# Kernel tuning notes

Hardware: AMD Instinct MI355X
Metric: run time of the kernel (lower is better)

The kernel has to match this reference:

```python
import jax, jax.numpy as jnp
import numpy as np

DECAY = 0.99
EPS_VQ = 1e-5
EPS_LN = 1e-5


def setup_inputs() -> dict:
    key = jax.random.key(0)
    ks = jax.random.split(key, 6)
    N, DIN, D, K = 32768, 1024, 512, 1024
    return {
        "x": jax.random.normal(ks[0], (N, DIN), dtype=jnp.float32),
        "enc_w": jax.random.normal(ks[1], (DIN, D), dtype=jnp.float32) * (1.0 / np.sqrt(DIN)),
        "enc_b": jnp.zeros((D,), jnp.float32),
        "ln_g": jnp.ones((D,), jnp.float32),
        "ln_b": jnp.zeros((D,), jnp.float32),
        "dec_w": jax.random.normal(ks[2], (D, DIN), dtype=jnp.float32) * (1.0 / np.sqrt(D)),
        "dec_b": jnp.zeros((DIN,), jnp.float32),
        "embeddings": jax.random.normal(ks[3], (K, D), dtype=jnp.float32),
        "cluster_size": jnp.ones((K,), jnp.float32),
        "ema_embed_sum": jax.random.normal(ks[4], (K, D), dtype=jnp.float32),
    }


def _layernorm(h, g, b):
    mu = jnp.mean(h, axis=-1, keepdims=True)
    var = jnp.var(h, axis=-1, keepdims=True)
    return (h - mu) * jax.lax.rsqrt(var + EPS_LN) * g + b


def reference(x, enc_w, enc_b, ln_g, ln_b, dec_w, dec_b, embeddings, cluster_size, ema_embed_sum):
    K = embeddings.shape[0]
    # encoder: Linear + LayerNorm
    z_e = _layernorm(x @ enc_w + enc_b, ln_g, ln_b)  # [N, D]
    # pairwise squared L2 distances, expanded GEMM form (same argmin as (z-e)^2.sum)
    d = (jnp.sum(z_e * z_e, axis=1, keepdims=True)
         - 2.0 * (z_e @ embeddings.T)
         + jnp.sum(embeddings * embeddings, axis=1)[None, :])  # [N, K]
    indices = jnp.argmin(d, axis=1)  # [N]
    z_q = embeddings[indices]  # gather [N, D]
    # EMA codebook update (training path; buffers, no grad)
    zd = jax.lax.stop_gradient(z_e)
    counts = jax.ops.segment_sum(jnp.ones_like(indices, jnp.float32), indices, num_segments=K)
    embed_sum = jax.ops.segment_sum(zd, indices, num_segments=K)  # one_hot.T @ z
    new_cluster_size = DECAY * cluster_size + (1.0 - DECAY) * counts
    new_ema_embed_sum = DECAY * ema_embed_sum + (1.0 - DECAY) * embed_sum
    n = jnp.sum(new_cluster_size)
    cs = (new_cluster_size + EPS_VQ) / (n + K * EPS_VQ) * n
    new_embeddings = new_ema_embed_sum / cs[:, None]
    # commitment loss + straight-through estimator
    commit_loss = jnp.mean((z_e - jax.lax.stop_gradient(z_q)) ** 2)
    z_q_st = z_e + jax.lax.stop_gradient(z_q - z_e)
    x_recon = z_q_st @ dec_w + dec_b
    return (x_recon, commit_loss, indices, z_e, z_q_st,
            new_embeddings, new_cluster_size, new_ema_embed_sum)
```

## Files before the change

kernel.cpp:

```cpp
#include <hip/hip_runtime.h>

typedef unsigned long long u64;
typedef unsigned int u32;
typedef _Float16 f16;
typedef _Float16 f16x8 __attribute__((ext_vector_type(8)));
typedef float f32x4 __attribute__((ext_vector_type(4)));

#define MFMA16(a, b, c) __builtin_amdgcn_mfma_f32_16x16x32_f16(a, b, c, 0, 0, 0)

#define NROWS 32768
#define DIN   1024
#define DM    512
#define KC    1024
#define SPLIT_SC  1024.0f
#define SPLIT_INV 0.0009765625f
#define CHSZ  32
#define MAXCH 2048
#define MARGIN 0.5f

#define OFF_XR   0ull
#define OFF_CL   33554432ull
#define OFF_IDX  33554433ull
#define OFF_ZE   33587201ull
#define OFF_ZQ   50364417ull
#define OFF_NE   67141633ull
#define OFF_NCS  67665921ull
#define OFF_NEMA 67666945ull

#define WS_ZNORM   2359296ull
#define WS_IDX     2490368ull
#define WS_COUNTS  2621440ull
#define WS_STARTS  2625536ull
#define WS_OFFW    2629632ull
#define WS_ROWLIST 2633728ull
#define WS_CSD     2764800ull
#define WS_ENORM   2769920ull
#define WS2_CAND   (4ull<<20)
#define WS2_WT1    (36ull<<20)
#define WS2_WT2    (37ull<<20)
#define WS2_DT     (38ull<<20)
#define WS2_E1     (39ull<<20)
#define WS3_CHPFX  (41ull<<20)
#define WS3_CHCODE ((41ull<<20) + 8192)
#define WS3_CPART  ((41ull<<20) + 16384)
#define WS3_PART   ((41ull<<20) + 65536)

__device__ inline void gload16(const f16* g, f16* l) {
  __builtin_amdgcn_global_load_lds((const __attribute__((address_space(1))) void*)g,
                                   (__attribute__((address_space(3))) void*)l, 16, 0, 0);
}

__device__ inline f16x8 ldfrag32(const f16* p, int row, int kc) {
  return *(const f16x8*)(p + row * 32 + ((kc ^ ((row >> 1) & 3)) << 3));
}

__device__ inline void stage32(const f16* gbase, int ld, int row0, int k0,
                               f16* lds, int t) {
  int r = t >> 2, c = t & 3;
  int cs = c ^ ((r >> 1) & 3);
  gload16(gbase + (size_t)(row0 + r) * ld + k0 + cs * 8, lds + t * 8);
}

__device__ inline void stageA256(const f16* gbase, int ld, int row0, int k0,
                                 f16* lds, int t) {
#pragma unroll
  for (int h = 0; h < 2; h++) {
    int e = t + h * 512;
    int r = e >> 2, c = e & 3;
    int cs = c ^ ((r >> 1) & 3);
    gload16(gbase + (size_t)(row0 + r) * ld + k0 + cs * 8, lds + e * 8);
  }
}

__device__ inline u32 enc_score(float s) {
  u32 kb = __float_as_uint(s);
  return (kb & 0x80000000u) ? ~kb : (kb | 0x80000000u);
}
__device__ inline float dec_score(u32 u) {
  u32 b = (u & 0x80000000u) ? (u & 0x7fffffffu) : ~u;
  return __uint_as_float(b);
}

__global__ __launch_bounds__(256) void k_prep(const float* __restrict__ enc_w,
                                              const float* __restrict__ dec_w,
                                              const float* __restrict__ emb,
                                              f16* __restrict__ wt1,
                                              f16* __restrict__ wt2,
                                              f16* __restrict__ dT,
                                              f16* __restrict__ e1,
                                              float* __restrict__ enorm,
                                              int* __restrict__ counts) {
  __shared__ float tile[32][33];
  int bid = blockIdx.x, t = threadIdx.x;
  if (bid < 1024) {
    const float* W;
    f16 *o1, *o2;
    int K, N, bx, by;
    if (bid < 512) {
      W = enc_w; o1 = wt1; o2 = wt2; K = DIN; N = DM;
      bx = bid & 15; by = bid >> 4;
    } else {
      int b2 = bid - 512;
      W = dec_w; o1 = dT; o2 = nullptr; K = DM; N = DIN;
      bx = b2 & 31; by = b2 >> 5;
    }
    int tx = t & 31, ty = t >> 5;
    int nb = bx * 32, kb = by * 32;
#pragma unroll
    for (int i = 0; i < 32; i += 8)
      tile[ty + i][tx] = W[(size_t)(kb + ty + i) * N + nb + tx];
    __syncthreads();
#pragma unroll
    for (int i = 0; i < 32; i += 8) {
      float v = tile[tx][ty + i];
      f16 h = (f16)v;
      size_t o = (size_t)(nb + ty + i) * K + kb + tx;
      o1[o] = h;
      if (o2) o2[o] = (f16)((v - (float)h) * SPLIT_SC);
    }
  } else if (bid < 1536) {
    int tid = (bid - 1024) * 256 + t;
    for (int i = tid; i < KC * DM; i += 131072) e1[i] = (f16)emb[i];
  } else if (bid < 1792) {
    int k = (bid - 1536) * 4 + (t >> 6), lane = t & 63;
    float s = 0.f;
#pragma unroll
    for (int j = 0; j < 8; j++) {
      float v = emb[(size_t)k * DM + lane + j * 64];
      s = fmaf(v, v, s);
    }
#pragma unroll
    for (int m = 1; m < 64; m <<= 1) s += __shfl_xor(s, m, 64);
    if (lane == 0) enorm[k] = s;
  } else {
    int i = (bid - 1792) * 256 + t;
    if (i < KC) counts[i] = 0;
  }
}

__global__ __launch_bounds__(512, 4) void k_genc6(const float* __restrict__ x,
                                                  const f16* __restrict__ wt1,
                                                  const f16* __restrict__ wt2,
                                                  const float* __restrict__ bias,
                                                  float* __restrict__ dst) {
  __shared__ __align__(16) f16 A1[2][128 * 32], A2[2][128 * 32];
  __shared__ __align__(16) f16 B1[2][128 * 32], B2[2][128 * 32];
  int t = threadIdx.x, lane = t & 63, wid = t >> 6;
  int wm = wid >> 2, wn = wid & 3;
  int l = blockIdx.x;
  int xcd = l & 7, s = l >> 3, ct = s & 3;
  int p = ((s >> 2) << 3) | xcd;
  int m0 = p * 128, n0 = ct * 128;
  int r = t >> 2, cg = t & 3;
  int cslot = cg ^ ((r >> 1) & 3);
  const float* ax = x + (size_t)(m0 + r) * DIN + cg * 8;
  f32x4 accA[4][2] = {}, accB[4][2] = {};

#define GCONV(v0, v1, buf)                                                  \
  {                                                                         \
    float a_[8] = {v0.x, v0.y, v0.z, v0.w, v1.x, v1.y, v1.z, v1.w};         \
    f16 h1_[8], h2_[8];                                                     \
    _Pragma("unroll") for (int j_ = 0; j_ < 8; j_++) {                      \
      f16 h_ = (f16)a_[j_];                                                 \
      h1_[j_] = h_;                                                         \
      h2_[j_] = (f16)((a_[j_] - (float)h_) * SPLIT_SC);                     \
    }                                                                       \
    *(f16x8*)(A1[buf] + r * 32 + cslot * 8) = *(f16x8*)h1_;                 \
    *(f16x8*)(A2[buf] + r * 32 + cslot * 8) = *(f16x8*)h2_;                 \
  }

#define GCOMP(buf)                                                          \
  {                                                                         \
    int kc_ = lane >> 4;                                                    \
    f16x8 a1f[4], a2f[4], b1f[2], b2f[2];                                   \
    _Pragma("unroll") for (int m_ = 0; m_ < 4; m_++) {                      \
      int row_ = wm * 64 + m_ * 16 + (lane & 15);                           \
      a1f[m_] = ldfrag32(A1[buf], row_, kc_);                               \
      a2f[m_] = ldfrag32(A2[buf], row_, kc_);                               \
    }                                                                       \
    _Pragma("unroll") for (int n_ = 0; n_ < 2; n_++) {                      \
      int row_ = wn * 32 + n_ * 16 + (lane & 15);                           \
      b1f[n_] = ldfrag32(B1[buf], row_, kc_);                               \
      b2f[n_] = ldfrag32(B2[buf], row_, kc_);                               \
    }                                                                       \
    _Pragma("unroll") for (int m_ = 0; m_ < 4; m_++)                        \
      _Pragma("unroll") for (int n_ = 0; n_ < 2; n_++) {                    \
        accA[m_][n_] = MFMA16(a1f[m_], b1f[n_], accA[m_][n_]);              \
        accB[m_][n_] = MFMA16(a1f[m_], b2f[n_], accB[m_][n_]);              \
        accB[m_][n_] = MFMA16(a2f[m_], b1f[n_], accB[m_][n_]);              \
      }                                                                     \
  }

  float4 c0 = *(const float4*)(ax);
  float4 c1 = *(const float4*)(ax + 4);
  stage32(wt1, DIN, n0, 0, B1[0], t);
  stage32(wt2, DIN, n0, 0, B2[0], t);
  float4 n0v = *(const float4*)(ax + 32);
  float4 n1v = *(const float4*)(ax + 36);
  asm volatile("s_waitcnt vmcnt(4)" ::: "memory");
  GCONV(c0, c1, 0);
  asm volatile("s_waitcnt vmcnt(2) lgkmcnt(0)" ::: "memory");
  __builtin_amdgcn_sched_barrier(0);
  __builtin_amdgcn_s_barrier();
  asm volatile("" ::: "memory");

  for (int it = 0; it < 32; ++it) {
    if (it + 1 < 32) {
      stage32(wt1, DIN, n0, (it + 1) * 32, B1[(it + 1) & 1], t);
      stage32(wt2, DIN, n0, (it + 1) * 32, B2[(it + 1) & 1], t);
    }
    float4 f0, f1;
    if (it + 2 < 32) {
      f0 = *(const float4*)(ax + (it + 2) * 32);
      f1 = *(const float4*)(ax + (it + 2) * 32 + 4);
    }
    GCOMP(it & 1);
    if (it + 1 < 32) {
      if (it <= 29) {
        asm volatile("s_waitcnt vmcnt(4)" ::: "memory");
      } else {
        asm volatile("s_waitcnt vmcnt(2)" ::: "memory");
      }
      GCONV(n0v, n1v, (it + 1) & 1);
      if (it <= 29) {
        asm volatile("s_waitcnt vmcnt(2) lgkmcnt(0)" ::: "memory");
      } else {
        asm volatile("s_waitcnt vmcnt(0) lgkmcnt(0)" ::: "memory");
      }
      __builtin_amdgcn_sched_barrier(0);
      __builtin_amdgcn_s_barrier();
      asm volatile("" ::: "memory");
    }
    n0v = f0; n1v = f1;
  }
#undef GCONV
#undef GCOMP

#pragma unroll
  for (int m = 0; m < 4; m++)
#pragma unroll
    for (int n = 0; n < 2; n++)
#pragma unroll
      for (int j = 0; j < 4; j++) {
        int row = m0 + wm * 64 + m * 16 + (lane >> 4) * 4 + j;
        int col = n0 + wn * 32 + n * 16 + (lane & 15);
        dst[(size_t)row * DM + col] = accA[m][n][j] + SPLIT_INV * accB[m][n][j] + bias[col];
      }
}

__global__ __launch_bounds__(512, 4) void k_dist4(const f16* __restrict__ z1,
                                                  const f16* __restrict__ e1,
                                                  const float* __restrict__ enorm,
                                                  u64* __restrict__ cand) {
  __shared__ __align__(16) f16 A[3][256 * 32];
  __shared__ __align__(16) f16 B[3][128 * 32];
  int t = threadIdx.x, lane = t & 63, wid = t >> 6;
  int wr = wid >> 1, wc = wid & 1;
  int l = blockIdx.x;
  int xcd = l & 7, s = l >> 3, ct = s & 7;
  int p = ((s >> 3) << 3) | xcd;
  int r0 = p * 256, c0 = ct * 128;
  f32x4 acc[4][4] = {};
  int kc = lane >> 4;

  stageA256(z1, DM, r0, 0, A[0], t);
  stage32(e1, DM, c0, 0, B[0], t);

  for (int it = 0; it < 16; ++it) {
    int buf = it % 3;
    if (it < 15) {
      int nb = (it + 1) % 3;
      int k0n = (it + 1) * 32;
      stageA256(z1, DM, r0, k0n, A[nb], t);
      stage32(e1, DM, c0, k0n, B[nb], t);
      asm volatile("s_waitcnt vmcnt(3)" ::: "memory");
    } else {
      asm volatile("s_waitcnt vmcnt(0)" ::: "memory");
    }
    __builtin_amdgcn_sched_barrier(0);
    __builtin_amdgcn_s_barrier();
    asm volatile("" ::: "memory");
    f16x8 af[4], bf[4];
#pragma unroll
    for (int m = 0; m < 4; m++)
      af[m] = ldfrag32(A[buf], wr * 64 + m * 16 + (lane & 15), kc);
#pragma unroll
    for (int n = 0; n < 4; n++)
      bf[n] = ldfrag32(B[buf], wc * 64 + n * 16 + (lane & 15), kc);
#pragma unroll
    for (int m = 0; m < 4; m++)
#pragma unroll
      for (int n = 0; n < 4; n++) acc[m][n] = MFMA16(af[m], bf[n], acc[m][n]);
  }

  __syncthreads();
  u64 (*cand_s)[4] = (u64 (*)[4])(&A[0][0]);
  float en[4];
#pragma unroll
  for (int n = 0; n < 4; n++)
    en[n] = enorm[c0 + wc * 64 + n * 16 + (lane & 15)];
#pragma unroll
  for (int m = 0; m < 4; m++)
#pragma unroll
    for (int j = 0; j < 4; j++) {
      int r_l = wr * 64 + m * 16 + (lane >> 4) * 4 + j;
      u64 lo = ~0ull, hi = ~0ull;
#pragma unroll
      for (int n = 0; n < 4; n++) {
        int col = c0 + wc * 64 + n * 16 + (lane & 15);
        float sc = fmaf(-2.0f, acc[m][n][j], en[n]);
        u64 k = ((u64)enc_score(sc) << 32) | (u32)col;
        if (k < lo) { hi = lo; lo = k; }
        else if (k < hi) { hi = k; }
      }
#pragma unroll
      for (int msk = 1; msk < 16; msk <<= 1) {
        u64 lo2 = __shfl_xor(lo, msk, 64);
        u64 hi2 = __shfl_xor(hi, msk, 64);
        u64 nlo = lo < lo2 ? lo : lo2;
        u64 losr = lo < lo2 ? lo2 : lo;
        u64 nh = hi < hi2 ? hi : hi2;
        hi = losr < nh ? losr : nh;
        lo = nlo;
      }
      if ((lane & 15) == 0) {
        cand_s[r_l][wc * 2] = lo;
        cand_s[r_l][wc * 2 + 1] = hi;
      }
    }
  __syncthreads();
  if (t < 256) {
    u64 b0 = ~0ull, b1 = ~0ull;
#pragma unroll
    for (int i = 0; i < 4; i++) {
      u64 k = cand_s[t][i];
      if (k < b0) { b1 = b0; b0 = k; }
      else if (k < b1) { b1 = k; }
    }
    u64* dst = cand + ((size_t)(r0 + t) * 16 + ct * 2);
    dst[0] = b0;
    dst[1] = b1;
  }
}

__global__ __launch_bounds__(512) void k_edgemm(const f16* __restrict__ e1,
                                                const f16* __restrict__ dT,
                                                const float* __restrict__ bias,
                                                float* __restrict__ ED) {
  __shared__ __align__(16) f16 A[3][128 * 32], B[3][128 * 32];
  int t = threadIdx.x, lane = t & 63, wid = t >> 6;
  int wm = wid >> 2, wn = wid & 3;
  int r0 = (blockIdx.x >> 3) * 128, c0 = (blockIdx.x & 7) * 128;
  f32x4 acc[4][2] = {};
  int kc = lane >> 4;

  stage32(e1, DM, r0, 0, A[0], t);
  stage32(dT, DM, c0, 0, B[0], t);

  for (int it = 0; it < 16; ++it) {
    int buf = it % 3;
    if (it < 15) {
      int nb = (it + 1) % 3;
      int k0n = (it + 1) * 32;
      stage32(e1, DM, r0, k0n, A[nb], t);
      stage32(dT, DM, c0, k0n, B[nb], t);
      asm volatile("s_waitcnt vmcnt(2)" ::: "memory");
    } else {
      asm volatile("s_waitcnt vmcnt(0)" ::: "memory");
    }
    __builtin_amdgcn_sched_barrier(0);
    __builtin_amdgcn_s_barrier();
    asm volatile("" ::: "memory");
    f16x8 af[4], bf[2];
#pragma unroll
    for (int m = 0; m < 4; m++)
      af[m] = ldfrag32(A[buf], wm * 64 + m * 16 + (lane & 15), kc);
#pragma unroll
    for (int n = 0; n < 2; n++)
      bf[n] = ldfrag32(B[buf], wn * 32 + n * 16 + (lane & 15), kc);
#pragma unroll
    for (int m = 0; m < 4; m++)
#pragma unroll
      for (int n = 0; n < 2; n++) acc[m][n] = MFMA16(af[m], bf[n], acc[m][n]);
  }

#pragma unroll
  for (int m = 0; m < 4; m++)
#pragma unroll
    for (int n = 0; n < 2; n++)
#pragma unroll
      for (int j = 0; j < 4; j++) {
        int row = r0 + wm * 64 + m * 16 + (lane >> 4) * 4 + j;
        int col = c0 + wn * 32 + n * 16 + (lane & 15);
        ED[(size_t)row * DIN + col] = acc[m][n][j] + bias[col];
      }
}

__global__ __launch_bounds__(256) void k_gatherx(const int* __restrict__ idxws,
                                                 const float* __restrict__ ED,
                                                 float* __restrict__ xr) {
  int t = threadIdx.x, r0 = blockIdx.x * 16;
  __shared__ int idx_s[16];
  if (t < 16) idx_s[t] = idxws[r0 + t];
  __syncthreads();
  for (int rr = 0; rr < 16; rr++) {
    int R = r0 + rr;
    const float4* src = (const float4*)(ED + (size_t)idx_s[rr] * DIN);
    float4* dst = (float4*)(xr + (size_t)R * DIN);
    dst[t] = src[t];
  }
}

__global__ __launch_bounds__(256) void k_resolve(const u64* __restrict__ cand,
                                                 const float* __restrict__ znorm,
                                                 const float* __restrict__ enorm,
                                                 const float* __restrict__ emb,
                                                 float* __restrict__ out,
                                                 int* __restrict__ idxws,
                                                 int* __restrict__ counts,
                                                 float* __restrict__ cpart) {
  int t = threadIdx.x, bid = blockIdx.x;
  int r0 = bid * 16;
  __shared__ u64 key_s[256];
  __shared__ int idx_s[16];
  __shared__ float commit_s[16];
  __shared__ int flagcnt_s;
  __shared__ int flagrow_s[16];
  key_s[t] = cand[(size_t)r0 * 16 + t];
  if (t == 0) flagcnt_s = 0;
  __syncthreads();

  if (t < 16) {
    u64 best = ~0ull;
#pragma unroll
    for (int i = 0; i < 16; i++) {
      u64 k = key_s[t * 16 + i];
      best = k < best ? k : best;
    }
    float smin = dec_score((u32)(best >> 32));
    float thr = smin + MARGIN;
    int nc = 0;
#pragma unroll
    for (int i = 0; i < 16; i++)
      if (dec_score((u32)(key_s[t * 16 + i] >> 32)) <= thr) nc++;
    idx_s[t] = (int)(u32)(best & 0xffffffffull);
    commit_s[t] = znorm[r0 + t] + smin;
    if (nc > 1) {
      int pz = atomicAdd(&flagcnt_s, 1);
      flagrow_s[pz] = t;
    }
  }
  __syncthreads();

  if (t < 64) {
    int nf = flagcnt_s;
    for (int fi = 0; fi < nf; fi++) {
      int lr = flagrow_s[fi];
      int R = r0 + lr;
      u64 amin = ~0ull;
      for (int i = 0; i < 16; i++) {
        u64 k = key_s[lr * 16 + i];
        amin = k < amin ? k : amin;
      }
      float thr = dec_score((u32)(amin >> 32)) + MARGIN;
      float zn = znorm[R];
      const float* z = out + OFF_ZE + (size_t)R * DM;
      u64 bestk = ~0ull;
      for (int i = 0; i < 16; i++) {
        u64 k = key_s[lr * 16 + i];
        if (dec_score((u32)(k >> 32)) > thr) continue;
        int c = (int)(u32)(k & 0xffffffffull);
        const float* e = emb + (size_t)c * DM;
        float pdot = 0.f;
#pragma unroll
        for (int j = 0; j < 8; j++) pdot = fmaf(z[t + j * 64], e[t + j * 64], pdot);
#pragma unroll
        for (int m = 1; m < 64; m <<= 1) pdot += __shfl_xor(pdot, m, 64);
        float d = fmaf(-2.0f, pdot, zn) + enorm[c];
        u64 pk = ((u64)enc_score(d) << 32) | (u32)c;
        bestk = pk < bestk ? pk : bestk;
      }
      if (t == 0) {
        idx_s[lr] = (int)(u32)(bestk & 0xffffffffull);
        commit_s[lr] = dec_score((u32)(bestk >> 32));
      }
    }
  }
  __syncthreads();

  if (t < 16) {
    int R = r0 + t;
    int idx = idx_s[t];
    out[OFF_IDX + R] = (float)idx;
    idxws[R] = idx;
    atomicAdd(counts + idx, 1);
  }
  __syncthreads();
  for (int rr = 0; rr < 16; rr++) {
    int R = r0 + rr;
    const float* e = emb + (size_t)idx_s[rr] * DM;
    float* zq = out + OFF_ZQ + (size_t)R * DM;
#pragma unroll
    for (int j = 0; j < 2; j++) {
      int c = t + j * 256;
      zq[c] = e[c];
    }
  }
  if (t == 0) {
    float s = 0.f;
#pragma unroll
    for (int i = 0; i < 16; i++) s += commit_s[i];
    cpart[bid] = s;
  }
}

__global__ __launch_bounds__(256) void k_ln3(float* __restrict__ ze,
                                             const float* __restrict__ g,
                                             const float* __restrict__ b,
                                             f16* __restrict__ z1,
                                             float* __restrict__ znorm) {
  int t = threadIdx.x, lane = t & 63, wid = t >> 6;
  int R = blockIdx.x * 4 + wid;
  float* row = ze + (size_t)R * DM;
  float v[8];
  float s = 0.f, sq = 0.f;
#pragma unroll
  for (int j = 0; j < 8; j++) {
    v[j] = row[lane + j * 64];
    s += v[j];
    sq = fmaf(v[j], v[j], sq);
  }
#pragma unroll
  for (int m = 1; m < 64; m <<= 1) {
    s += __shfl_xor(s, m, 64);
    sq += __shfl_xor(sq, m, 64);
  }
  float mu = s * (1.f / DM);
  float var = sq * (1.f / DM) - mu * mu;
  float rs = rsqrtf(var + 1e-5f);
  float zn = 0.f;
#pragma unroll
  for (int j = 0; j < 8; j++) {
    int c = lane + j * 64;
    float o = (v[j] - mu) * rs * g[c] + b[c];
    row[c] = o;
    z1[(size_t)R * DM + c] = (f16)o;
    zn = fmaf(o, o, zn);
  }
#pragma unroll
  for (int m = 1; m < 64; m <<= 1) zn += __shfl_xor(zn, m, 64);
  if (lane == 0) znorm[R] = zn;
}

__global__ __launch_bounds__(1024) void k_scan(const int* __restrict__ counts,
                                               const float* __restrict__ cs_in,
                                               float* __restrict__ out,
                                               int* __restrict__ starts,
                                               int* __restrict__ offw,
                                               float* __restrict__ csd,
                                               const float* __restrict__ cpart,
                                               int* __restrict__ chpfx,
                                               int* __restrict__ chcode) {
  __shared__ float f[1024];
  __shared__ int ib[1024];
  int t = threadIdx.x;
  f[t] = cpart[t] + cpart[t + 1024];
  __syncthreads();
  for (int s = 512; s > 0; s >>= 1) {
    if (t < s) f[t] += f[t + s];
    __syncthreads();
  }
  if (t == 0) out[OFF_CL] = f[0] * (1.f / ((float)NROWS * (float)DM));
  __syncthreads();

  int cnt = counts[t];
  float ncs = 0.99f * cs_in[t] + 0.01f * (float)cnt;
  out[OFF_NCS + t] = ncs;
  f[t] = ncs;
  __syncthreads();
  for (int s = 512; s > 0; s >>= 1) {
    if (t < s) f[t] += f[t + s];
    __syncthreads();
  }
  float n = f[0];
  csd[t] = (ncs + 1e-5f) / (n + (float)KC * 1e-5f) * n;
  ib[t] = cnt;
  __syncthreads();
  for (int s = 1; s < 1024; s <<= 1) {
    int y = (t >= s) ? ib[t - s] : 0;
    __syncthreads();
    ib[t] += y;
    __syncthreads();
  }
  int excl = ib[t] - cnt;
  starts[t] = excl;
  offw[t] = excl;
  int nch = (cnt + CHSZ - 1) / CHSZ;
  __syncthreads();
  ib[t] = nch;
  __syncthreads();
  for (int s = 1; s < 1024; s <<= 1) {
    int y = (t >= s) ? ib[t - s] : 0;
    __syncthreads();
    ib[t] += y;
    __syncthreads();
  }
  int chx = ib[t] - nch;
  chpfx[t] = chx;
  if (t == KC - 1) chpfx[KC] = ib[t];
  for (int j = 0; j < nch; j++) chcode[chx + j] = t;
}

__global__ __launch_bounds__(256) void k_scatter(const int* __restrict__ idxws,
                                                 int* __restrict__ offw,
                                                 int* __restrict__ rowlist) {
  int r = blockIdx.x * 256 + threadIdx.x;
  int idx = idxws[r];
  int pos = atomicAdd(offw + idx, 1);
  rowlist[pos] = r;
}

__global__ __launch_bounds__(128) void k_partsum(const int* __restrict__ chpfx,
                                                 const int* __restrict__ chcode,
                                                 const int* __restrict__ starts,
                                                 const int* __restrict__ counts,
                                                 const int* __restrict__ rowlist,
                                                 const float* __restrict__ out,
                                                 float* __restrict__ part) {
  int c = blockIdx.x, t = threadIdx.x;
  if (c >= chpfx[KC]) return;
  int code = chcode[c];
  int j = c - chpfx[code];
  int ofs = starts[code] + j * CHSZ;
  int len = min(CHSZ, counts[code] - j * CHSZ);
  __shared__ int rl[CHSZ];
  if (t < len) rl[t] = rowlist[ofs + t];
  __syncthreads();
  const float* zeb = out + OFF_ZE;
  float a0 = 0.f, a1 = 0.f, a2 = 0.f, a3 = 0.f;
  for (int i = 0; i < len; i++) {
    const float* z = zeb + (size_t)rl[i] * DM;
    a0 += z[t];
    a1 += z[t + 128];
    a2 += z[t + 256];
    a3 += z[t + 384];
  }
  float* pp = part + (size_t)c * DM;
  pp[t] = a0;
  pp[t + 128] = a1;
  pp[t + 256] = a2;
  pp[t + 384] = a3;
}

__global__ __launch_bounds__(128) void k_codesum2(const int* __restrict__ chpfx,
                                                  const float* __restrict__ part,
                                                  const float* __restrict__ ema_in,
                                                  const float* __restrict__ csd,
                                                  float* __restrict__ out) {
  int k = blockIdx.x, t = threadIdx.x;
  int base = chpfx[k], nch = chpfx[k + 1] - base;
  float a0 = 0.f, a1 = 0.f, a2 = 0.f, a3 = 0.f;
  for (int i = 0; i < nch; i++) {
    const float* pp = part + (size_t)(base + i) * DM;
    a0 += pp[t];
    a1 += pp[t + 128];
    a2 += pp[t + 256];
    a3 += pp[t + 384];
  }
  float cs = csd[k];
  float sum[4] = {a0, a1, a2, a3};
#pragma unroll
  for (int j = 0; j < 4; j++) {
    int c = t + j * 128;
    float e = 0.99f * ema_in[(size_t)k * DM + c] + 0.01f * sum[j];
    out[OFF_NEMA + (size_t)k * DM + c] = e;
    out[OFF_NE + (size_t)k * DM + c] = e / cs;
  }
}

extern "C" void kernel_launch(void* const* d_in, const int* in_sizes, int n_in,
                              void* d_out, int out_size, void* d_ws, size_t ws_size,
                              hipStream_t stream) {
  (void)in_sizes; (void)n_in; (void)out_size; (void)ws_size;
  const float* x = (const float*)d_in[0];
  const float* enc_w = (const float*)d_in[1];
  const float* enc_b = (const float*)d_in[2];
  const float* ln_g = (const float*)d_in[3];
  const float* ln_b = (const float*)d_in[4];
  const float* dec_w = (const float*)d_in[5];
  const float* dec_b = (const float*)d_in[6];
  const float* emb = (const float*)d_in[7];
  const float* cs_in = (const float*)d_in[8];
  const float* ema_in = (const float*)d_in[9];
  float* out = (float*)d_out;
  char* ws = (char*)d_ws;
  float* znorm = (float*)(ws + WS_ZNORM);
  int* idxws = (int*)(ws + WS_IDX);
  int* counts = (int*)(ws + WS_COUNTS);
  int* starts = (int*)(ws + WS_STARTS);
  int* offw = (int*)(ws + WS_OFFW);
  int* rowlist = (int*)(ws + WS_ROWLIST);
  float* csd = (float*)(ws + WS_CSD);
  float* enorm = (float*)(ws + WS_ENORM);
  u64* cand = (u64*)(ws + WS2_CAND);
  float* ED = (float*)(ws + WS2_CAND);
  f16* wt1 = (f16*)(ws + WS2_WT1);
  f16* wt2 = (f16*)(ws + WS2_WT2);
  f16* dT = (f16*)(ws + WS2_DT);
  f16* e1 = (f16*)(ws + WS2_E1);
  int* chpfx = (int*)(ws + WS3_CHPFX);
  int* chcode = (int*)(ws + WS3_CHCODE);
  float* cpart = (float*)(ws + WS3_CPART);
  float* part = (float*)(ws + WS3_PART);
  f16* z1 = (f16*)out;

  k_prep<<<dim3(1796), dim3(256), 0, stream>>>(enc_w, dec_w, emb, wt1, wt2, dT,
                                               e1, enorm, counts);
  k_genc6<<<dim3(1024), dim3(512), 0, stream>>>(x, wt1, wt2, enc_b, out + OFF_ZE);
  k_ln3<<<dim3(8192), dim3(256), 0, stream>>>(out + OFF_ZE, ln_g, ln_b, z1, znorm);
  k_dist4<<<dim3(1024), dim3(512), 0, stream>>>(z1, e1, enorm, cand);
  k_resolve<<<dim3(2048), dim3(256), 0, stream>>>(cand, znorm, enorm, emb, out,
                                                  idxws, counts, cpart);
  k_edgemm<<<dim3(64), dim3(512), 0, stream>>>(e1, dT, dec_b, ED);
  k_scan<<<dim3(1), dim3(1024), 0, stream>>>(counts, cs_in, out, starts, offw, csd,
                                             cpart, chpfx, chcode);
  k_scatter<<<dim3(NROWS / 256), dim3(256), 0, stream>>>(idxws, offw, rowlist);
  k_partsum<<<dim3(MAXCH), dim3(128), 0, stream>>>(chpfx, chcode, starts, counts,
                                                   rowlist, out, part);
  k_codesum2<<<dim3(KC), dim3(128), 0, stream>>>(chpfx, part, ema_in, csd, out);
  k_gatherx<<<dim3(2048), dim3(256), 0, stream>>>(idxws, ED, out + OFF_XR);
}
```

Baseline: 331.7 us.

## Triple-buffer encoder weight tiles and retile distance GEMM to fewer column tiles

The encoder GEMM now triple-buffers the B (weight) tiles, issuing loads two iterations ahead so weight fetches are hidden behind more compute. The distance kernel swaps its tile shape from 256 rows by 128 codes to 128 rows by 256 codes. Each row therefore yields 8 candidate keys instead of 16, and the resolve kernel and scan partial sums are resized to match. This cuts candidate write and read traffic and resolve work. The cost is more LDS per block and a different reuse balance in the distance GEMM.

```diff
diff --git a/kernel.cpp b/kernel.cpp
--- a/kernel.cpp
+++ b/kernel.cpp
@@ -138,13 +138,13 @@
   }
 }
 
-__global__ __launch_bounds__(512, 4) void k_genc6(const float* __restrict__ x,
+__global__ __launch_bounds__(512, 4) void k_genc7(const float* __restrict__ x,
                                                   const f16* __restrict__ wt1,
                                                   const f16* __restrict__ wt2,
                                                   const float* __restrict__ bias,
                                                   float* __restrict__ dst) {
   __shared__ __align__(16) f16 A1[2][128 * 32], A2[2][128 * 32];
-  __shared__ __align__(16) f16 B1[2][128 * 32], B2[2][128 * 32];
+  __shared__ __align__(16) f16 B1[3][128 * 32], B2[3][128 * 32];
   int t = threadIdx.x, lane = t & 63, wid = t >> 6;
   int wm = wid >> 2, wn = wid & 3;
   int l = blockIdx.x;
@@ -169,19 +169,19 @@
     *(f16x8*)(A2[buf] + r * 32 + cslot * 8) = *(f16x8*)h2_;                 \
   }
 
-#define GCOMP(buf)                                                          \
+#define GCOMP(abuf, bbuf)                                                   \
   {                                                                         \
     int kc_ = lane >> 4;                                                    \
     f16x8 a1f[4], a2f[4], b1f[2], b2f[2];                                   \
     _Pragma("unroll") for (int m_ = 0; m_ < 4; m_++) {                      \
       int row_ = wm * 64 + m_ * 16 + (lane & 15);                           \
-      a1f[m_] = ldfrag32(A1[buf], row_, kc_);                               \
-      a2f[m_] = ldfrag32(A2[buf], row_, kc_);                               \
+      a1f[m_] = ldfrag32(A1[abuf], row_, kc_);                              \
+      a2f[m_] = ldfrag32(A2[abuf], row_, kc_);                              \
     }                                                                       \
     _Pragma("unroll") for (int n_ = 0; n_ < 2; n_++) {                      \
       int row_ = wn * 32 + n_ * 16 + (lane & 15);                           \
-      b1f[n_] = ldfrag32(B1[buf], row_, kc_);                               \
-      b2f[n_] = ldfrag32(B2[buf], row_, kc_);                               \
+      b1f[n_] = ldfrag32(B1[bbuf], row_, kc_);                              \
+      b2f[n_] = ldfrag32(B2[bbuf], row_, kc_);                              \
     }                                                                       \
     _Pragma("unroll") for (int m_ = 0; m_ < 4; m_++)                        \
       _Pragma("unroll") for (int n_ = 0; n_ < 2; n_++) {                    \
@@ -191,42 +191,38 @@
       }                                                                     \
   }
 
+  stage32(wt1, DIN, n0, 0, B1[0], t);
+  stage32(wt2, DIN, n0, 0, B2[0], t);
   float4 c0 = *(const float4*)(ax);
   float4 c1 = *(const float4*)(ax + 4);
-  stage32(wt1, DIN, n0, 0, B1[0], t);
-  stage32(wt2, DIN, n0, 0, B2[0], t);
+  stage32(wt1, DIN, n0, 32, B1[1], t);
+  stage32(wt2, DIN, n0, 32, B2[1], t);
   float4 n0v = *(const float4*)(ax + 32);
   float4 n1v = *(const float4*)(ax + 36);
   asm volatile("s_waitcnt vmcnt(4)" ::: "memory");
   GCONV(c0, c1, 0);
-  asm volatile("s_waitcnt vmcnt(2) lgkmcnt(0)" ::: "memory");
+  asm volatile("s_waitcnt lgkmcnt(0)" ::: "memory");
   __builtin_amdgcn_sched_barrier(0);
   __builtin_amdgcn_s_barrier();
   asm volatile("" ::: "memory");
 
   for (int it = 0; it < 32; ++it) {
-    if (it + 1 < 32) {
-      stage32(wt1, DIN, n0, (it + 1) * 32, B1[(it + 1) & 1], t);
-      stage32(wt2, DIN, n0, (it + 1) * 32, B2[(it + 1) & 1], t);
-    }
     float4 f0, f1;
     if (it + 2 < 32) {
+      stage32(wt1, DIN, n0, (it + 2) * 32, B1[(it + 2) % 3], t);
+      stage32(wt2, DIN, n0, (it + 2) * 32, B2[(it + 2) % 3], t);
       f0 = *(const float4*)(ax + (it + 2) * 32);
       f1 = *(const float4*)(ax + (it + 2) * 32 + 4);
     }
-    GCOMP(it & 1);
+    GCOMP(it & 1, it % 3);
     if (it + 1 < 32) {
       if (it <= 29) {
         asm volatile("s_waitcnt vmcnt(4)" ::: "memory");
       } else {
-        asm volatile("s_waitcnt vmcnt(2)" ::: "memory");
+        asm volatile("s_waitcnt vmcnt(0)" ::: "memory");
       }
       GCONV(n0v, n1v, (it + 1) & 1);
-      if (it <= 29) {
-        asm volatile("s_waitcnt vmcnt(2) lgkmcnt(0)" ::: "memory");
-      } else {
-        asm volatile("s_waitcnt vmcnt(0) lgkmcnt(0)" ::: "memory");
-      }
+      asm volatile("s_waitcnt lgkmcnt(0)" ::: "memory");
       __builtin_amdgcn_sched_barrier(0);
       __builtin_amdgcn_s_barrier();
       asm volatile("" ::: "memory");
@@ -248,31 +244,31 @@
       }
 }
 
-__global__ __launch_bounds__(512, 4) void k_dist4(const f16* __restrict__ z1,
+__global__ __launch_bounds__(512, 4) void k_dist5(const f16* __restrict__ z1,
                                                   const f16* __restrict__ e1,
                                                   const float* __restrict__ enorm,
                                                   u64* __restrict__ cand) {
-  __shared__ __align__(16) f16 A[3][256 * 32];
-  __shared__ __align__(16) f16 B[3][128 * 32];
+  __shared__ __align__(16) f16 A[3][128 * 32];
+  __shared__ __align__(16) f16 B[3][256 * 32];
   int t = threadIdx.x, lane = t & 63, wid = t >> 6;
-  int wr = wid >> 1, wc = wid & 1;
+  int wr = wid >> 2, wc = wid & 3;
   int l = blockIdx.x;
-  int xcd = l & 7, s = l >> 3, ct = s & 7;
-  int p = ((s >> 3) << 3) | xcd;
-  int r0 = p * 256, c0 = ct * 128;
+  int xcd = l & 7, s = l >> 3, ct = s & 3;
+  int p = ((s >> 2) << 3) | xcd;
+  int r0 = p * 128, c0 = ct * 256;
   f32x4 acc[4][4] = {};
   int kc = lane >> 4;
 
-  stageA256(z1, DM, r0, 0, A[0], t);
-  stage32(e1, DM, c0, 0, B[0], t);
+  stage32(z1, DM, r0, 0, A[0], t);
+  stageA256(e1, DM, c0, 0, B[0], t);
 
   for (int it = 0; it < 16; ++it) {
     int buf = it % 3;
     if (it < 15) {
       int nb = (it + 1) % 3;
       int k0n = (it + 1) * 32;
-      stageA256(z1, DM, r0, k0n, A[nb], t);
-      stage32(e1, DM, c0, k0n, B[nb], t);
+      stage32(z1, DM, r0, k0n, A[nb], t);
+      stageA256(e1, DM, c0, k0n, B[nb], t);
       asm volatile("s_waitcnt vmcnt(3)" ::: "memory");
     } else {
       asm volatile("s_waitcnt vmcnt(0)" ::: "memory");
@@ -294,7 +290,7 @@
   }
 
   __syncthreads();
-  u64 (*cand_s)[4] = (u64 (*)[4])(&A[0][0]);
+  u64 (*cand_s)[8] = (u64 (*)[8])(&A[0][0]);
   float en[4];
 #pragma unroll
   for (int n = 0; n < 4; n++)
@@ -329,17 +325,120 @@
       }
     }
   __syncthreads();
-  if (t < 256) {
+  if (t < 128) {
     u64 b0 = ~0ull, b1 = ~0ull;
 #pragma unroll
-    for (int i = 0; i < 4; i++) {
+    for (int i = 0; i < 8; i++) {
       u64 k = cand_s[t][i];
       if (k < b0) { b1 = b0; b0 = k; }
       else if (k < b1) { b1 = k; }
     }
-    u64* dst = cand + ((size_t)(r0 + t) * 16 + ct * 2);
+    u64* dst = cand + ((size_t)(r0 + t) * 8 + ct * 2);
     dst[0] = b0;
     dst[1] = b1;
+  }
+}
+
+__global__ __launch_bounds__(256) void k_resolve5(const u64* __restrict__ cand,
+                                                  const float* __restrict__ znorm,
+                                                  const float* __restrict__ enorm,
+                                                  const float* __restrict__ emb,
+                                                  float* __restrict__ out,
+                                                  int* __restrict__ idxws,
+                                                  int* __restrict__ counts,
+                                                  float* __restrict__ cpart) {
+  int t = threadIdx.x, bid = blockIdx.x;
+  int r0 = bid * 32;
+  __shared__ u64 key_s[256];
+  __shared__ int idx_s[32];
+  __shared__ float commit_s[32];
+  __shared__ int flagcnt_s;
+  __shared__ int flagrow_s[32];
+  key_s[t] = cand[(size_t)r0 * 8 + t];
+  if (t == 0) flagcnt_s = 0;
+  __syncthreads();
+
+  if (t < 32) {
+    u64 best = ~0ull;
+#pragma unroll
+    for (int i = 0; i < 8; i++) {
+      u64 k = key_s[t * 8 + i];
+      best = k < best ? k : best;
+    }
+    float smin = dec_score((u32)(best >> 32));
+    float thr = smin + MARGIN;
+    int nc = 0;
+#pragma unroll
+    for (int i = 0; i < 8; i++)
+      if (dec_score((u32)(key_s[t * 8 + i] >> 32)) <= thr) nc++;
+    idx_s[t] = (int)(u32)(best & 0xffffffffull);
+    commit_s[t] = znorm[r0 + t] + smin;
+    if (nc > 1) {
+      int pz = atomicAdd(&flagcnt_s, 1);
+      flagrow_s[pz] = t;
+    }
+  }
+  __syncthreads();
+
+  if (t < 64) {
+    int nf = flagcnt_s;
+    for (int fi = 0; fi < nf; fi++) {
+      int lr = flagrow_s[fi];
+      int R = r0 + lr;
+      u64 amin = ~0ull;
+      for (int i = 0; i < 8; i++) {
+        u64 k = key_s[lr * 8 + i];
+        amin = k < amin ? k : amin;
+      }
+      float thr = dec_score((u32)(amin >> 32)) + MARGIN;
+      float zn = znorm[R];
+      const float* z = out + OFF_ZE + (size_t)R * DM;
+      u64 bestk = ~0ull;
+      for (int i = 0; i < 8; i++) {
+        u64 k = key_s[lr * 8 + i];
+        if (dec_score((u32)(k >> 32)) > thr) continue;
+        int c = (int)(u32)(k & 0xffffffffull);
+        const float* e = emb + (size_t)c * DM;
+        float pdot = 0.f;
+#pragma unroll
+        for (int j = 0; j < 8; j++) pdot = fmaf(z[t + j * 64], e[t + j * 64], pdot);
+#pragma unroll
+        for (int m = 1; m < 64; m <<= 1) pdot += __shfl_xor(pdot, m, 64);
+        float d = fmaf(-2.0f, pdot, zn) + enorm[c];
+        u64 pk = ((u64)enc_score(d) << 32) | (u32)c;
+        bestk = pk < bestk ? pk : bestk;
+      }
+      if (t == 0) {
+        idx_s[lr] = (int)(u32)(bestk & 0xffffffffull);
+        commit_s[lr] = dec_score((u32)(bestk >> 32));
+      }
+    }
+  }
+  __syncthreads();
+
+  if (t < 32) {
+    int R = r0 + t;
+    int idx = idx_s[t];
+    out[OFF_IDX + R] = (float)idx;
+    idxws[R] = idx;
+    atomicAdd(counts + idx, 1);
+  }
+  __syncthreads();
+  for (int rr = 0; rr < 32; rr++) {
+    int R = r0 + rr;
+    const float* e = emb + (size_t)idx_s[rr] * DM;
+    float* zq = out + OFF_ZQ + (size_t)R * DM;
+#pragma unroll
+    for (int j = 0; j < 2; j++) {
+      int c = t + j * 256;
+      zq[c] = e[c];
+    }
+  }
+  if (t == 0) {
+    float s = 0.f;
+#pragma unroll
+    for (int i = 0; i < 32; i++) s += commit_s[i];
+    cpart[bid] = s;
   }
 }
 
@@ -408,109 +507,6 @@
     const float4* src = (const float4*)(ED + (size_t)idx_s[rr] * DIN);
     float4* dst = (float4*)(xr + (size_t)R * DIN);
     dst[t] = src[t];
-  }
-}
-
-__global__ __launch_bounds__(256) void k_resolve(const u64* __restrict__ cand,
-                                                 const float* __restrict__ znorm,
-                                                 const float* __restrict__ enorm,
-                                                 const float* __restrict__ emb,
-                                                 float* __restrict__ out,
-                                                 int* __restrict__ idxws,
-                                                 int* __restrict__ counts,
-                                                 float* __restrict__ cpart) {
-  int t = threadIdx.x, bid = blockIdx.x;
-  int r0 = bid * 16;
-  __shared__ u64 key_s[256];
-  __shared__ int idx_s[16];
-  __shared__ float commit_s[16];
-  __shared__ int flagcnt_s;
-  __shared__ int flagrow_s[16];
-  key_s[t] = cand[(size_t)r0 * 16 + t];
-  if (t == 0) flagcnt_s = 0;
-  __syncthreads();
-
-  if (t < 16) {
-    u64 best = ~0ull;
-#pragma unroll
-    for (int i = 0; i < 16; i++) {
-      u64 k = key_s[t * 16 + i];
-      best = k < best ? k : best;
-    }
-    float smin = dec_score((u32)(best >> 32));
-    float thr = smin + MARGIN;
-    int nc = 0;
-#pragma unroll
-    for (int i = 0; i < 16; i++)
-      if (dec_score((u32)(key_s[t * 16 + i] >> 32)) <= thr) nc++;
-    idx_s[t] = (int)(u32)(best & 0xffffffffull);
-    commit_s[t] = znorm[r0 + t] + smin;
-    if (nc > 1) {
-      int pz = atomicAdd(&flagcnt_s, 1);
-      flagrow_s[pz] = t;
-    }
-  }
-  __syncthreads();
-
-  if (t < 64) {
-    int nf = flagcnt_s;
-    for (int fi = 0; fi < nf; fi++) {
-      int lr = flagrow_s[fi];
-      int R = r0 + lr;
-      u64 amin = ~0ull;
-      for (int i = 0; i < 16; i++) {
-        u64 k = key_s[lr * 16 + i];
-        amin = k < amin ? k : amin;
-      }
-      float thr = dec_score((u32)(amin >> 32)) + MARGIN;
-      float zn = znorm[R];
-      const float* z = out + OFF_ZE + (size_t)R * DM;
-      u64 bestk = ~0ull;
-      for (int i = 0; i < 16; i++) {
-        u64 k = key_s[lr * 16 + i];
-        if (dec_score((u32)(k >> 32)) > thr) continue;
-        int c = (int)(u32)(k & 0xffffffffull);
-        const float* e = emb + (size_t)c * DM;
-        float pdot = 0.f;
-#pragma unroll
-        for (int j = 0; j < 8; j++) pdot = fmaf(z[t + j * 64], e[t + j * 64], pdot);
-#pragma unroll
-        for (int m = 1; m < 64; m <<= 1) pdot += __shfl_xor(pdot, m, 64);
-        float d = fmaf(-2.0f, pdot, zn) + enorm[c];
-        u64 pk = ((u64)enc_score(d) << 32) | (u32)c;
-        bestk = pk < bestk ? pk : bestk;
-      }
-      if (t == 0) {
-        idx_s[lr] = (int)(u32)(bestk & 0xffffffffull);
-        commit_s[lr] = dec_score((u32)(bestk >> 32));
-      }
-    }
-  }
-  __syncthreads();
-
-  if (t < 16) {
-    int R = r0 + t;
-    int idx = idx_s[t];
-    out[OFF_IDX + R] = (float)idx;
-    idxws[R] = idx;
-    atomicAdd(counts + idx, 1);
-  }
-  __syncthreads();
-  for (int rr = 0; rr < 16; rr++) {
-    int R = r0 + rr;
-    const float* e = emb + (size_t)idx_s[rr] * DM;
-    float* zq = out + OFF_ZQ + (size_t)R * DM;
-#pragma unroll
-    for (int j = 0; j < 2; j++) {
-      int c = t + j * 256;
-      zq[c] = e[c];
-    }
-  }
-  if (t == 0) {
-    float s = 0.f;
-#pragma unroll
-    for (int i = 0; i < 16; i++) s += commit_s[i];
-    cpart[bid] = s;
   }
 }
 
@@ -564,7 +560,7 @@
   __shared__ float f[1024];
   __shared__ int ib[1024];
   int t = threadIdx.x;
-  f[t] = cpart[t] + cpart[t + 1024];
+  f[t] = cpart[t];
   __syncthreads();
   for (int s = 512; s > 0; s >>= 1) {
     if (t < s) f[t] += f[t + s];
@@ -716,11 +712,11 @@
 
   k_prep<<<dim3(1796), dim3(256), 0, stream>>>(enc_w, dec_w, emb, wt1, wt2, dT,
                                                e1, enorm, counts);
-  k_genc6<<<dim3(1024), dim3(512), 0, stream>>>(x, wt1, wt2, enc_b, out + OFF_ZE);
+  k_genc7<<<dim3(1024), dim3(512), 0, stream>>>(x, wt1, wt2, enc_b, out + OFF_ZE);
   k_ln3<<<dim3(8192), dim3(256), 0, stream>>>(out + OFF_ZE, ln_g, ln_b, z1, znorm);
-  k_dist4<<<dim3(1024), dim3(512), 0, stream>>>(z1, e1, enorm, cand);
-  k_resolve<<<dim3(2048), dim3(256), 0, stream>>>(cand, znorm, enorm, emb, out,
-                                                  idxws, counts, cpart);
+  k_dist5<<<dim3(1024), dim3(512), 0, stream>>>(z1, e1, enorm, cand);
+  k_resolve5<<<dim3(1024), dim3(256), 0, stream>>>(cand, znorm, enorm, emb, out,
+                                                   idxws, counts, cpart);
   k_edgemm<<<dim3(64), dim3(512), 0, stream>>>(e1, dT, dec_b, ED);
   k_scan<<<dim3(1), dim3(1024), 0, stream>>>(counts, cs_in, out, starts, offw, csd,
                                              cpart, chpfx, chcode);
```

New measurement: 329.6 us. About the same (-0.6%).
